# Kernel optimization log

Hardware: AMD Instinct MI355X
Metric: run time of the kernel (lower is better)

## Reference

```python
import jax, jax.numpy as jnp
import numpy as np

EPS = 1e-8
N_ITER = 3
S = 8      # n_slots
D = 64     # slot_size
HID = 128  # mlp hidden


def _ln(x, w, b):
    m = jnp.mean(x, axis=-1, keepdims=True)
    v = jnp.var(x, axis=-1, keepdims=True)
    return (x - m) * jax.lax.rsqrt(v + 1e-5) * w + b


def setup_inputs() -> dict:
    key = jax.random.key(0)
    ks = jax.random.split(key, 20)
    B, N, Din = 128, 4096, 64
    g = lambda k, sh, s: (jax.random.normal(k, sh, jnp.float32) * s)
    return {
        "inputs": jax.random.normal(ks[0], (B, N, Din), jnp.float32),
        "eps_noise": jax.random.normal(ks[1], (B, S, D), jnp.float32),
        "slot_mu": g(ks[2], (1, 1, D), 0.1),
        "slot_logvar": g(ks[3], (1, 1, D), 0.1),
        "k_w": g(ks[4], (D, Din), 1.0 / np.sqrt(Din)),
        "v_w": g(ks[5], (D, Din), 1.0 / np.sqrt(Din)),
        "q_w": g(ks[6], (D, D), 1.0 / np.sqrt(D)),
        "ni_w": jnp.ones((Din,), jnp.float32), "ni_b": jnp.zeros((Din,), jnp.float32),
        "ns_w": jnp.ones((D,), jnp.float32),  "ns_b": jnp.zeros((D,), jnp.float32),
        "nr_w": jnp.ones((D,), jnp.float32),  "nr_b": jnp.zeros((D,), jnp.float32),
        "gru_wih": g(ks[7], (3 * D, D), 1.0 / np.sqrt(D)),
        "gru_whh": g(ks[8], (3 * D, D), 1.0 / np.sqrt(D)),
        "gru_bih": jnp.zeros((3 * D,), jnp.float32),
        "gru_bhh": jnp.zeros((3 * D,), jnp.float32),
        "mlp_w1": g(ks[9], (HID, D), 1.0 / np.sqrt(D)),
        "mlp_w2": g(ks[10], (D, HID), 1.0 / np.sqrt(HID)),
        "mlp_b2": jnp.zeros((D,), jnp.float32),
    }


def _gru(x, h, wih, whh, bih, bhh):
    gi = x @ wih.T + bih  # [BS, 3D]
    gh = h @ whh.T + bhh
    i_r, i_z, i_n = jnp.split(gi, 3, axis=-1)
    h_r, h_z, h_n = jnp.split(gh, 3, axis=-1)
    r = jax.nn.sigmoid(i_r + h_r)
    z = jax.nn.sigmoid(i_z + h_z)
    n = jnp.tanh(i_n + r * h_n)
    return (1.0 - z) * n + z * h


def _step(slots, k, v, q_w, ns_w, ns_b, nr_w, nr_b,
          gru_wih, gru_whh, gru_bih, gru_bhh, mlp_w1, mlp_w2, mlp_b2):
    B = slots.shape[0]
    q = _ln(slots, ns_w, ns_b) @ q_w.T                     # [B,S,D]
    logits = jnp.einsum('bnd,bsd->bns', k, q)              # [B,N,S]
    w = jax.nn.softmax(logits, axis=-1) + EPS              # softmax over slots
    w = w / jnp.sum(w, axis=-2, keepdims=True)             # renorm over tokens
    atten_maps = jnp.einsum('bns,bnd->bsd', w, v)          # [B,S,D]
    h = _gru(atten_maps.reshape(B * S, D), slots.reshape(B * S, D),
             gru_wih, gru_whh, gru_bih, gru_bhh)
    h = h + (jax.nn.relu(_ln(h, nr_w, nr_b) @ mlp_w1.T) @ mlp_w2.T + mlp_b2)
    return h.reshape(B, S, D), w


def reference(inputs, eps_noise, slot_mu, slot_logvar, k_w, v_w, q_w,
              ni_w, ni_b, ns_w, ns_b, nr_w, nr_b,
              gru_wih, gru_whh, gru_bih, gru_bhh, mlp_w1, mlp_w2, mlp_b2):
    std = jnp.exp(0.5 * slot_logvar)
    slots = slot_mu + std * eps_noise                      # [B,S,D]
    x = _ln(inputs, ni_w, ni_b)
    k = (x @ k_w.T) / np.sqrt(D).astype(np.float32)        # [B,N,D]
    v = x @ v_w.T
    args = (q_w, ns_w, ns_b, nr_w, nr_b, gru_wih, gru_whh,
            gru_bih, gru_bhh, mlp_w1, mlp_w2, mlp_b2)
    for _ in range(N_ITER):
        slots, w = _step(slots, k, v, *args)
    slots, w = _step(jax.lax.stop_gradient(slots), k, v, *args)
    return slots, w
```

## Files before the change

### kernel.cpp

```cpp
#include <hip/hip_runtime.h>
#include <hip/hip_bf16.h>

#define BB 128
#define NN 4096
#define DD 64
#define SS 8
#define HH 128

typedef __attribute__((ext_vector_type(8))) short short8;
typedef __attribute__((ext_vector_type(4))) short short4v;
typedef __attribute__((ext_vector_type(4))) float f32x4;

__device__ __forceinline__ float warp_red_sum(float v) {
    #pragma unroll
    for (int off = 32; off; off >>= 1) v += __shfl_xor(v, off);
    return v;
}

__device__ __forceinline__ float bcastlane(float v, int l) {
    return __int_as_float(__builtin_amdgcn_readlane(__float_as_int(v), l));
}

__device__ __forceinline__ unsigned short bfu(float f) {
    __hip_bfloat16 h = __float2bfloat16(f);
    return *(unsigned short*)&h;
}

__device__ __forceinline__ unsigned pk2(float a, float b) {
    return (unsigned)bfu(a) | ((unsigned)bfu(b) << 16);
}

__global__ __launch_bounds__(256) void prep_kernel(
    const float* __restrict__ v_w, const float* __restrict__ q_w,
    const float* __restrict__ wih, const float* __restrict__ whh,
    const float* __restrict__ w1, const float* __restrict__ w2,
    float* __restrict__ vwT, float* __restrict__ qwT,
    float* __restrict__ wihT, float* __restrict__ whhT,
    float* __restrict__ w1T, float* __restrict__ w2T)
{
    int i0 = blockIdx.x * blockDim.x + threadIdx.x;
    int nthr = gridDim.x * blockDim.x;
    for (int t = i0; t < 4096; t += nthr) {
        int i = t >> 6, o = t & 63;
        vwT[t] = v_w[o * 64 + i];
        qwT[t] = q_w[o * 64 + i];
    }
    for (int t = i0; t < 12288; t += nthr) {
        int r = t / 192, c = t % 192;
        wihT[t] = wih[c * 64 + r];
        whhT[t] = whh[c * 64 + r];
    }
    for (int t = i0; t < 8192; t += nthr) {
        int r = t >> 7, c = t & 127;
        w1T[t] = w1[c * 64 + r];
    }
    for (int t = i0; t < 8192; t += nthr) {
        int r = t >> 6, c = t & 63;
        w2T[t] = w2[c * 128 + r];
    }
}

__global__ __launch_bounds__(256) void init_q_kernel(
    const float* __restrict__ eps, const float* __restrict__ mu,
    const float* __restrict__ lv, const float* __restrict__ qwT,
    const float* __restrict__ k_w,
    const float* __restrict__ nsw, const float* __restrict__ nsb,
    float* __restrict__ slots, unsigned short* __restrict__ qb,
    float* __restrict__ zbuf)
{
    const int tid = threadIdx.x, lane = tid & 63;
    const int row = blockIdx.x * 4 + (tid >> 6);
    const int idx = row * 64 + lane;
    float s0 = mu[lane] + __expf(0.5f * lv[lane]) * eps[idx];
    slots[idx] = s0;
    float m = warp_red_sum(s0) * (1.0f / 64.0f);
    float dx = s0 - m;
    float var = warp_red_sum(dx * dx) * (1.0f / 64.0f);
    float xln = dx * rsqrtf(var + 1e-5f) * nsw[lane] + nsb[lane];
    float q = 0.f;
    #pragma unroll 8
    for (int i = 0; i < 64; ++i) q = fmaf(bcastlane(xln, i), qwT[i * 64 + lane], q);
    float qp = 0.f;
    #pragma unroll 8
    for (int o = 0; o < 64; ++o) qp = fmaf(bcastlane(q, o), k_w[o * 64 + lane], qp);
    qb[idx] = bfu(qp * 0.125f);
    int g = blockIdx.x * 256 + tid;
    for (int j = g; j < 66560; j += 65536) zbuf[j] = 0.f;
}

__global__ __launch_bounds__(256) void phase_a_ln(
    const float* __restrict__ inp, const float* __restrict__ niw, const float* __restrict__ nib,
    unsigned short* __restrict__ xb)
{
    const int tid = threadIdx.x, lane = tid & 63, widx = tid >> 6;
    const int t8 = lane >> 3, d8 = lane & 7;
    const float4 wn0 = *(const float4*)&niw[d8 * 8];
    const float4 wn1 = *(const float4*)&niw[d8 * 8 + 4];
    const float4 bn0 = *(const float4*)&nib[d8 * 8];
    const float4 bn1 = *(const float4*)&nib[d8 * 8 + 4];
    const int tok0 = blockIdx.x * 128;
    #pragma unroll
    for (int it = 0; it < 4; ++it) {
        const int m = widx * 32 + it * 8 + t8;
        const float* rowp = inp + (size_t)(tok0 + m) * 64 + d8 * 8;
        float4 a = *(const float4*)rowp;
        float4 c = *(const float4*)(rowp + 4);
        float s1 = (a.x + a.y + a.z + a.w) + (c.x + c.y + c.z + c.w);
        float s2 = fmaf(a.x, a.x, fmaf(a.y, a.y, fmaf(a.z, a.z, a.w * a.w)));
        s2 = fmaf(c.x, c.x, fmaf(c.y, c.y, fmaf(c.z, c.z, fmaf(c.w, c.w, s2))));
        #pragma unroll
        for (int o = 1; o < 8; o <<= 1) { s1 += __shfl_xor(s1, o); s2 += __shfl_xor(s2, o); }
        float mean = s1 * (1.0f / 64.0f);
        float var = s2 * (1.0f / 64.0f) - mean * mean;
        float rstd = rsqrtf(var + 1e-5f);
        float y[8];
        y[0] = (a.x - mean) * rstd * wn0.x + bn0.x;
        y[1] = (a.y - mean) * rstd * wn0.y + bn0.y;
        y[2] = (a.z - mean) * rstd * wn0.z + bn0.z;
        y[3] = (a.w - mean) * rstd * wn0.w + bn0.w;
        y[4] = (c.x - mean) * rstd * wn1.x + bn1.x;
        y[5] = (c.y - mean) * rstd * wn1.y + bn1.y;
        y[6] = (c.z - mean) * rstd * wn1.z + bn1.z;
        y[7] = (c.w - mean) * rstd * wn1.w + bn1.w;
        uint4 o4;
        o4.x = pk2(y[0], y[1]); o4.y = pk2(y[2], y[3]);
        o4.z = pk2(y[4], y[5]); o4.w = pk2(y[6], y[7]);
        *(uint4*)&xb[(size_t)(tok0 + m) * 64 + d8 * 8] = o4;
    }
}

__global__ __launch_bounds__(256) void attn_mfma(
    const __hip_bfloat16* __restrict__ xb,
    const unsigned short* __restrict__ qb,
    float* __restrict__ numer, float* __restrict__ denom, float* __restrict__ wout)
{
    __shared__ unsigned short smem[14976];
    unsigned short* Qs = smem;
    const int tid = threadIdx.x, lane = tid & 63, widx = tid >> 6;
    unsigned short* wls = smem + 1152 + widx * 1152;
    unsigned short* Xw  = smem + 5760 + widx * 2304;
    const int b = blockIdx.y;

    for (int t = tid; t < 1024; t += 256) {
        int s = t >> 6, dd = t & 63;
        Qs[s * 72 + dd] = (s < 8) ? qb[b * 512 + t] : (unsigned short)0;
    }
    for (int t = lane; t < 576; t += 64) wls[576 + t] = 0;
    __syncthreads();

    const int quad = lane >> 4, l16 = lane & 15;
    short8 aq0 = *(const short8*)&Qs[l16 * 72 + quad * 8];
    short8 aq1 = *(const short8*)&Qs[l16 * 72 + 32 + quad * 8];

    f32x4 accv[4];
    #pragma unroll
    for (int nt = 0; nt < 4; ++nt) accv[nt] = (f32x4){0.f, 0.f, 0.f, 0.f};
    float dacc[4] = {0.f, 0.f, 0.f, 0.f};

    const int twave0 = blockIdx.x * 512 + widx * 128;
    #pragma unroll
    for (int iter = 0; iter < 2; ++iter) {
        const int t0 = twave0 + iter * 64;
        short8 bk[4][2];
        #pragma unroll
        for (int t4 = 0; t4 < 4; ++t4) {
            const size_t xrow = ((size_t)b * NN + t0 + t4 * 16 + l16) * 64;
            bk[t4][0] = *(const short8*)&xb[xrow + quad * 8];
            bk[t4][1] = *(const short8*)&xb[xrow + 32 + quad * 8];
        }
        #pragma unroll
        for (int h = 0; h < 2; ++h) {
            #pragma unroll
            for (int t4h = 0; t4h < 2; ++t4h) {
                const int t4 = h * 2 + t4h;
                const int tok = t0 + t4 * 16 + l16;
                const int tl = t4h * 16 + l16;
                short8 bk0 = bk[t4][0];
                short8 bk1 = bk[t4][1];
                #pragma unroll
                for (int j = 0; j < 8; ++j) {
                    Xw[(quad * 8 + j) * 36 + tl]      = (unsigned short)bk0[j];
                    Xw[(32 + quad * 8 + j) * 36 + tl] = (unsigned short)bk1[j];
                }
                f32x4 lg = (f32x4){0.f, 0.f, 0.f, 0.f};
                lg = __builtin_amdgcn_mfma_f32_16x16x32_bf16(aq0, bk0, lg, 0, 0, 0);
                lg = __builtin_amdgcn_mfma_f32_16x16x32_bf16(aq1, bk1, lg, 0, 0, 0);
                float e[4];
                #pragma unroll
                for (int r = 0; r < 4; ++r) e[r] = __expf(lg[r]);
                float s4 = (e[0] + e[1]) + (e[2] + e[3]);
                float stot = s4 + __shfl_xor(s4, 16);
                float rs = __builtin_amdgcn_rcpf(stot);
                float wv[4];
                #pragma unroll
                for (int r = 0; r < 4; ++r) { wv[r] = fmaf(e[r], rs, 1e-8f); dacc[r] += wv[r]; }
                if (quad < 2) {
                    #pragma unroll
                    for (int r = 0; r < 4; ++r)
                        wls[(quad * 4 + r) * 72 + t4 * 16 + l16] = bfu(wv[r]);
                    if (wout)
                        *(float4*)&wout[((size_t)b * NN + tok) * 8 + quad * 4] =
                            make_float4(wv[0], wv[1], wv[2], wv[3]);
                }
            }
            short8 aw = *(const short8*)&wls[l16 * 72 + h * 32 + quad * 8];
            #pragma unroll
            for (int nt = 0; nt < 4; ++nt) {
                const unsigned short* Xr = Xw + (nt * 16 + l16) * 36 + quad * 8;
                short4v lo = *(const short4v*)Xr;
                short4v hi = *(const short4v*)(Xr + 4);
                short8 bv;
                bv[0] = lo[0]; bv[1] = lo[1]; bv[2] = lo[2]; bv[3] = lo[3];
                bv[4] = hi[0]; bv[5] = hi[1]; bv[6] = hi[2]; bv[7] = hi[3];
                accv[nt] = __builtin_amdgcn_mfma_f32_16x16x32_bf16(aw, bv, accv[nt], 0, 0, 0);
            }
        }
    }
    #pragma unroll
    for (int r = 0; r < 4; ++r) {
        dacc[r] += __shfl_xor(dacc[r], 1);
        dacc[r] += __shfl_xor(dacc[r], 2);
        dacc[r] += __shfl_xor(dacc[r], 4);
        dacc[r] += __shfl_xor(dacc[r], 8);
    }
    __syncthreads();
    float* red = (float*)smem;
    float* dred = red + 2048;
    if (quad < 2) {
        #pragma unroll
        for (int nt = 0; nt < 4; ++nt)
            #pragma unroll
            for (int r = 0; r < 4; ++r)
                red[widx * 512 + (quad * 4 + r) * 64 + nt * 16 + l16] = accv[nt][r];
        if (l16 == 0) {
            #pragma unroll
            for (int r = 0; r < 4; ++r) dred[widx * 8 + quad * 4 + r] = dacc[r];
        }
    }
    __syncthreads();
    for (int e = tid; e < 512; e += 256)
        atomicAdd(numer + (size_t)b * 512 + e, red[e] + red[512 + e] + red[1024 + e] + red[1536 + e]);
    if (tid < 8)
        atomicAdd(denom + b * 8 + tid, dred[tid] + dred[8 + tid] + dred[16 + tid] + dred[24 + tid]);
}

__global__ __launch_bounds__(256) void gru_q_kernel(
    const float* __restrict__ numerX, const float* __restrict__ denom,
    const float* __restrict__ slotsIn,
    const float* __restrict__ vwT, const float* __restrict__ wihT, const float* __restrict__ whhT,
    const float* __restrict__ w1T, const float* __restrict__ w2T,
    const float* __restrict__ bih, const float* __restrict__ bhh,
    const float* __restrict__ nrw, const float* __restrict__ nrb,
    const float* __restrict__ b2,
    const float* __restrict__ qwT, const float* __restrict__ k_w,
    const float* __restrict__ nsw, const float* __restrict__ nsb,
    float* __restrict__ slotsOut, unsigned short* __restrict__ qb,
    float* __restrict__ zbuf)
{
    const int tid = threadIdx.x, lane = tid & 63;
    const int row = blockIdx.x * 4 + (tid >> 6);
    float nx = numerX[row * 64 + lane];
    float xp = 0.f;
    #pragma unroll 8
    for (int i = 0; i < 64; ++i) xp = fmaf(bcastlane(nx, i), vwT[i * 64 + lane], xp);
    float x = xp / denom[row];
    float h = slotsIn[row * 64 + lane];
    float air = 0, aiz = 0, ain = 0, ahr = 0, ahz = 0, ahn = 0;
    #pragma unroll 8
    for (int i = 0; i < 64; ++i) {
        float xi = bcastlane(x, i), hi = bcastlane(h, i);
        const float* wi = wihT + i * 192;
        const float* wh = whhT + i * 192;
        air = fmaf(xi, wi[lane], air);
        aiz = fmaf(xi, wi[64 + lane], aiz);
        ain = fmaf(xi, wi[128 + lane], ain);
        ahr = fmaf(hi, wh[lane], ahr);
        ahz = fmaf(hi, wh[64 + lane], ahz);
        ahn = fmaf(hi, wh[128 + lane], ahn);
    }
    air += bih[lane]; aiz += bih[64 + lane]; ain += bih[128 + lane];
    ahr += bhh[lane]; ahz += bhh[64 + lane]; ahn += bhh[128 + lane];
    float r = 1.f / (1.f + __expf(-(air + ahr)));
    float z = 1.f / (1.f + __expf(-(aiz + ahz)));
    float n = tanhf(ain + r * ahn);
    float hn = (1.f - z) * n + z * h;
    float m = warp_red_sum(hn) * (1.0f / 64.0f);
    float dx = hn - m;
    float var = warp_red_sum(dx * dx) * (1.0f / 64.0f);
    float u = dx * rsqrtf(var + 1e-5f) * nrw[lane] + nrb[lane];
    float o0 = 0.f, o1 = 0.f;
    #pragma unroll 8
    for (int i = 0; i < 64; ++i) {
        float ui = bcastlane(u, i);
        const float* w1r = w1T + i * 128;
        o0 = fmaf(ui, w1r[lane], o0);
        o1 = fmaf(ui, w1r[64 + lane], o1);
    }
    o0 = fmaxf(o0, 0.f); o1 = fmaxf(o1, 0.f);
    float y = 0.f;
    #pragma unroll 8
    for (int j = 0; j < 64; ++j) y = fmaf(bcastlane(o0, j), w2T[j * 64 + lane], y);
    #pragma unroll 8
    for (int j = 0; j < 64; ++j) y = fmaf(bcastlane(o1, j), w2T[(64 + j) * 64 + lane], y);
    y += b2[lane];
    float out = hn + y;
    slotsOut[row * 64 + lane] = out;
    float m2 = warp_red_sum(out) * (1.0f / 64.0f);
    float dx2 = out - m2;
    float var2 = warp_red_sum(dx2 * dx2) * (1.0f / 64.0f);
    float u2 = dx2 * rsqrtf(var2 + 1e-5f) * nsw[lane] + nsb[lane];
    float q = 0.f;
    #pragma unroll 8
    for (int i = 0; i < 64; ++i) q = fmaf(bcastlane(u2, i), qwT[i * 64 + lane], q);
    float qp = 0.f;
    #pragma unroll 8
    for (int o = 0; o < 64; ++o) qp = fmaf(bcastlane(q, o), k_w[o * 64 + lane], qp);
    qb[row * 64 + lane] = bfu(qp * 0.125f);
    int g = blockIdx.x * 256 + tid;
    for (int j = g; j < 66560; j += 65536) zbuf[j] = 0.f;
}

__global__ __launch_bounds__(256) void renorm_kernel(float* __restrict__ wout,
                                                     const float* __restrict__ denom)
{
    const size_t i4 = (size_t)blockIdx.x * blockDim.x + threadIdx.x;
    const size_t b = i4 >> 13;
    const int half = (int)(i4 & 1);
    float4 v = reinterpret_cast<float4*>(wout)[i4];
    const float4 dv = reinterpret_cast<const float4*>(denom)[b * 2 + half];
    v.x /= dv.x; v.y /= dv.y; v.z /= dv.z; v.w /= dv.w;
    reinterpret_cast<float4*>(wout)[i4] = v;
}

extern "C" void kernel_launch(void* const* d_in, const int* in_sizes, int n_in,
                              void* d_out, int out_size, void* d_ws, size_t ws_size,
                              hipStream_t stream)
{
    const float* inputs  = (const float*)d_in[0];
    const float* eps_n   = (const float*)d_in[1];
    const float* mu      = (const float*)d_in[2];
    const float* lv      = (const float*)d_in[3];
    const float* k_w     = (const float*)d_in[4];
    const float* v_w     = (const float*)d_in[5];
    const float* q_w     = (const float*)d_in[6];
    const float* ni_w    = (const float*)d_in[7];
    const float* ni_b    = (const float*)d_in[8];
    const float* ns_w    = (const float*)d_in[9];
    const float* ns_b    = (const float*)d_in[10];
    const float* nr_w    = (const float*)d_in[11];
    const float* nr_b    = (const float*)d_in[12];
    const float* gru_wih = (const float*)d_in[13];
    const float* gru_whh = (const float*)d_in[14];
    const float* gru_bih = (const float*)d_in[15];
    const float* gru_bhh = (const float*)d_in[16];
    const float* mlp_w1  = (const float*)d_in[17];
    const float* mlp_w2  = (const float*)d_in[18];
    const float* mlp_b2  = (const float*)d_in[19];

    char* wsb = (char*)d_ws;
    unsigned short* xb  = (unsigned short*)wsb;
    float* f      = (float*)(wsb + 134217728);
    float* slotsA = f;
    float* slotsB = f + 65536;
    unsigned short* qb = (unsigned short*)(f + 131072);
    float* numer0 = f + 163840;
    float* denom0 = f + 229376;
    float* numer1 = f + 230400;
    float* denom1 = f + 295936;
    float* vwT    = f + 296960;
    float* qwT    = f + 301056;
    float* wihT   = f + 305152;
    float* whhT   = f + 317440;
    float* w1T    = f + 329728;
    float* w2T    = f + 337920;

    float* out_slots = (float*)d_out;
    float* out_w     = out_slots + 65536;

    prep_kernel<<<64, 256, 0, stream>>>(v_w, q_w, gru_wih, gru_whh, mlp_w1, mlp_w2,
                                        vwT, qwT, wihT, whhT, w1T, w2T);
    init_q_kernel<<<256, 256, 0, stream>>>(eps_n, mu, lv, qwT, k_w, ns_w, ns_b,
                                           slotsA, qb, numer0);
    phase_a_ln<<<4096, 256, 0, stream>>>(inputs, ni_w, ni_b, xb);

    float* cur = slotsA;
    float* numers[2] = {numer0, numer1};
    float* denoms[2] = {denom0, denom1};
    for (int step = 0; step < 4; ++step) {
        int pb = step & 1;
        attn_mfma<<<dim3(8, 128), 256, 0, stream>>>((const __hip_bfloat16*)xb, qb,
                                                    numers[pb], denoms[pb],
                                                    step == 3 ? out_w : nullptr);
        float* nxt = (step == 3) ? out_slots : ((step & 1) ? slotsA : slotsB);
        gru_q_kernel<<<256, 256, 0, stream>>>(numers[pb], denoms[pb], cur,
                                              vwT, wihT, whhT, w1T, w2T,
                                              gru_bih, gru_bhh, nr_w, nr_b, mlp_b2,
                                              qwT, k_w, ns_w, ns_b,
                                              nxt, qb, numers[1 - pb]);
        cur = nxt;
    }
    renorm_kernel<<<4096, 256, 0, stream>>>(out_w, denom1);
}
```

Before: 392.8 us.

## Use LDS transpose reads and double-buffered prefetch in attention MFMA kernel

```diff
diff --git a/kernel.cpp b/kernel.cpp
--- a/kernel.cpp
+++ b/kernel.cpp
@@ -28,6 +28,12 @@
 
 __device__ __forceinline__ unsigned pk2(float a, float b) {
     return (unsigned)bfu(a) | ((unsigned)bfu(b) << 16);
+}
+
+__device__ __forceinline__ short4v ds_tr16(unsigned off) {
+    short4v r;
+    asm volatile("ds_read_b64_tr_b16 %0, %1" : "=v"(r) : "v"(off));
+    return r;
 }
 
 __global__ __launch_bounds__(256) void prep_kernel(
@@ -134,21 +140,30 @@
     const unsigned short* __restrict__ qb,
     float* __restrict__ numer, float* __restrict__ denom, float* __restrict__ wout)
 {
-    __shared__ unsigned short smem[14976];
+    __shared__ unsigned short smem[11904];
     unsigned short* Qs = smem;
     const int tid = threadIdx.x, lane = tid & 63, widx = tid >> 6;
-    unsigned short* wls = smem + 1152 + widx * 1152;
-    unsigned short* Xw  = smem + 5760 + widx * 2304;
+    unsigned short* wls = smem + 1152 + widx * 640;
+    unsigned short* Xw  = smem + 3712 + widx * 2048;
     const int b = blockIdx.y;
+    const int quad = lane >> 4, l16 = lane & 15;
+    const int twave0 = blockIdx.x * 512 + widx * 128;
+
+    short8 bkA[2][2], bkB[2][2];
+    #pragma unroll
+    for (int t4h = 0; t4h < 2; ++t4h) {
+        const size_t xrow = ((size_t)b * NN + twave0 + t4h * 16 + l16) * 64;
+        bkA[t4h][0] = *(const short8*)&xb[xrow + quad * 8];
+        bkA[t4h][1] = *(const short8*)&xb[xrow + 32 + quad * 8];
+    }
 
     for (int t = tid; t < 1024; t += 256) {
         int s = t >> 6, dd = t & 63;
         Qs[s * 72 + dd] = (s < 8) ? qb[b * 512 + t] : (unsigned short)0;
     }
-    for (int t = lane; t < 576; t += 64) wls[576 + t] = 0;
+    for (int t = lane; t < 320; t += 64) wls[320 + t] = 0;
     __syncthreads();
 
-    const int quad = lane >> 4, l16 = lane & 15;
     short8 aq0 = *(const short8*)&Qs[l16 * 72 + quad * 8];
     short8 aq1 = *(const short8*)&Qs[l16 * 72 + 32 + quad * 8];
 
@@ -157,65 +172,70 @@
     for (int nt = 0; nt < 4; ++nt) accv[nt] = (f32x4){0.f, 0.f, 0.f, 0.f};
     float dacc[4] = {0.f, 0.f, 0.f, 0.f};
 
-    const int twave0 = blockIdx.x * 512 + widx * 128;
-    #pragma unroll
-    for (int iter = 0; iter < 2; ++iter) {
-        const int t0 = twave0 + iter * 64;
-        short8 bk[4][2];
-        #pragma unroll
-        for (int t4 = 0; t4 < 4; ++t4) {
-            const size_t xrow = ((size_t)b * NN + t0 + t4 * 16 + l16) * 64;
-            bk[t4][0] = *(const short8*)&xb[xrow + quad * 8];
-            bk[t4][1] = *(const short8*)&xb[xrow + 32 + quad * 8];
+    unsigned short* xw0 = Xw + (quad >> 1) * 512 + l16 * 16 + (quad & 1) * 8;
+    const unsigned xtr = (unsigned)(size_t)Xw
+                       + (unsigned)((quad * 8 + (l16 >> 2)) * 32 + (l16 & 3) * 8);
+
+    auto PROC = [&](short8 (&cur)[2][2], short8 (&nxt)[2][2], int hg, bool pf) {
+        const int t0g = twave0 + hg * 32;
+        if (pf) {
+            #pragma unroll
+            for (int t4h = 0; t4h < 2; ++t4h) {
+                const size_t xrow = ((size_t)b * NN + t0g + 32 + t4h * 16 + l16) * 64;
+                nxt[t4h][0] = *(const short8*)&xb[xrow + quad * 8];
+                nxt[t4h][1] = *(const short8*)&xb[xrow + 32 + quad * 8];
+            }
         }
         #pragma unroll
-        for (int h = 0; h < 2; ++h) {
+        for (int t4h = 0; t4h < 2; ++t4h) {
+            const int tok = t0g + t4h * 16 + l16;
+            short8 bk0 = cur[t4h][0];
+            short8 bk1 = cur[t4h][1];
+            *(short8*)(xw0 + t4h * 256) = bk0;
+            *(short8*)(xw0 + t4h * 256 + 1024) = bk1;
+            f32x4 lg = (f32x4){0.f, 0.f, 0.f, 0.f};
+            lg = __builtin_amdgcn_mfma_f32_16x16x32_bf16(aq0, bk0, lg, 0, 0, 0);
+            lg = __builtin_amdgcn_mfma_f32_16x16x32_bf16(aq1, bk1, lg, 0, 0, 0);
+            float e[4];
             #pragma unroll
-            for (int t4h = 0; t4h < 2; ++t4h) {
-                const int t4 = h * 2 + t4h;
-                const int tok = t0 + t4 * 16 + l16;
-                const int tl = t4h * 16 + l16;
-                short8 bk0 = bk[t4][0];
-                short8 bk1 = bk[t4][1];
+            for (int r = 0; r < 4; ++r) e[r] = __expf(lg[r]);
+            float s4 = (e[0] + e[1]) + (e[2] + e[3]);
+            float stot = s4 + __shfl_xor(s4, 16);
+            float rs = __builtin_amdgcn_rcpf(stot);
+            float wv[4];
+            #pragma unroll
+            for (int r = 0; r < 4; ++r) { wv[r] = fmaf(e[r], rs, 1e-8f); dacc[r] += wv[r]; }
+            if (quad < 2) {
                 #pragma unroll
-                for (int j = 0; j < 8; ++j) {
-                    Xw[(quad * 8 + j) * 36 + tl]      = (unsigned short)bk0[j];
-                    Xw[(32 + quad * 8 + j) * 36 + tl] = (unsigned short)bk1[j];
-                }
-                f32x4 lg = (f32x4){0.f, 0.f, 0.f, 0.f};
-                lg = __builtin_amdgcn_mfma_f32_16x16x32_bf16(aq0, bk0, lg, 0, 0, 0);
-                lg = __builtin_amdgcn_mfma_f32_16x16x32_bf16(aq1, bk1, lg, 0, 0, 0);
-                float e[4];
-                #pragma unroll
-                for (int r = 0; r < 4; ++r) e[r] = __expf(lg[r]);
-                float s4 = (e[0] + e[1]) + (e[2] + e[3]);
-                float stot = s4 + __shfl_xor(s4, 16);
-                float rs = __builtin_amdgcn_rcpf(stot);
-                float wv[4];
-                #pragma unroll
-                for (int r = 0; r < 4; ++r) { wv[r] = fmaf(e[r], rs, 1e-8f); dacc[r] += wv[r]; }
-                if (quad < 2) {
-                    #pragma unroll
-                    for (int r = 0; r < 4; ++r)
-                        wls[(quad * 4 + r) * 72 + t4 * 16 + l16] = bfu(wv[r]);
-                    if (wout)
-                        *(float4*)&wout[((size_t)b * NN + tok) * 8 + quad * 4] =
-                            make_float4(wv[0], wv[1], wv[2], wv[3]);
-                }
-            }
-            short8 aw = *(const short8*)&wls[l16 * 72 + h * 32 + quad * 8];
-            #pragma unroll
-            for (int nt = 0; nt < 4; ++nt) {
-                const unsigned short* Xr = Xw + (nt * 16 + l16) * 36 + quad * 8;
-                short4v lo = *(const short4v*)Xr;
-                short4v hi = *(const short4v*)(Xr + 4);
-                short8 bv;
-                bv[0] = lo[0]; bv[1] = lo[1]; bv[2] = lo[2]; bv[3] = lo[3];
-                bv[4] = hi[0]; bv[5] = hi[1]; bv[6] = hi[2]; bv[7] = hi[3];
-                accv[nt] = __builtin_amdgcn_mfma_f32_16x16x32_bf16(aw, bv, accv[nt], 0, 0, 0);
+                for (int r = 0; r < 4; ++r)
+                    wls[(quad * 4 + r) * 40 + t4h * 16 + l16] = bfu(wv[r]);
+                if (wout)
+                    *(float4*)&wout[((size_t)b * NN + tok) * 8 + quad * 4] =
+                        make_float4(wv[0], wv[1], wv[2], wv[3]);
             }
         }
-    }
+        asm volatile("" ::: "memory");
+        short8 aw = *(const short8*)&wls[l16 * 40 + quad * 8];
+        short4v rlo[4], rhi[4];
+        #pragma unroll
+        for (int nt = 0; nt < 4; ++nt) {
+            rlo[nt] = ds_tr16(xtr + nt * 1024);
+            rhi[nt] = ds_tr16(xtr + nt * 1024 + 128);
+        }
+        asm volatile("s_waitcnt lgkmcnt(0)");
+        __builtin_amdgcn_sched_barrier(0);
+        #pragma unroll
+        for (int nt = 0; nt < 4; ++nt) {
+            short8 bv = __builtin_shufflevector(rlo[nt], rhi[nt], 0, 1, 2, 3, 4, 5, 6, 7);
+            accv[nt] = __builtin_amdgcn_mfma_f32_16x16x32_bf16(aw, bv, accv[nt], 0, 0, 0);
+        }
+    };
+
+    PROC(bkA, bkB, 0, true);
+    PROC(bkB, bkA, 1, true);
+    PROC(bkA, bkB, 2, true);
+    PROC(bkB, bkA, 3, false);
+
     #pragma unroll
     for (int r = 0; r < 4; ++r) {
         dacc[r] += __shfl_xor(dacc[r], 1);
```

Result: no change. 390.3 us (-0.6%).
